# Kernel tuning notes

Measured on AMD Instinct MI355X. Metric: run time of the kernel, lower is better.

Reference implementation:

```python
import jax, jax.numpy as jnp
import numpy as np

N_PATHS, N_LINKS, L, DEG, D = 50000, 10000, 8, 40, 64
ITERS = 8
# (min, scale) pairs from override_min_max_scores
MM_FT = (0.0, 1e-4); MM_FP = (0.0, 1e-3); MM_FPS = (0.0, 1e-3); MM_LC = (0.0, 1e-5)


def _gru(x, h, wx, wh, bx, bh):
    # Keras GRUCell (reset_after=True, tanh/sigmoid)
    mx = x @ wx + bx
    mh = h @ wh + bh
    xz, xr, xh = jnp.split(mx, 3, axis=-1)
    rz, rr, rh = jnp.split(mh, 3, axis=-1)
    z = jax.nn.sigmoid(xz + rz)
    r = jax.nn.sigmoid(xr + rr)
    hh = jnp.tanh(xh + r * rh)
    return z * h + (1.0 - z) * hh


def setup_inputs():
    key = jax.random.key(0)
    ks = jax.random.split(key, 30)
    w = lambda k, s: jax.random.normal(k, s, jnp.float32) * 0.05
    inp = {
        'flow_traffic': jax.random.uniform(ks[0], (N_PATHS, 1), jnp.float32, 100.0, 10000.0),
        'flow_packets': jax.random.uniform(ks[1], (N_PATHS, 1), jnp.float32, 1.0, 1000.0),
        'flow_packet_size': jax.random.uniform(ks[2], (N_PATHS, 1), jnp.float32, 100.0, 1500.0),
        'link_capacity': jax.random.uniform(ks[3], (N_LINKS, 1), jnp.float32, 1.0, 100.0),
        'link_to_path': jax.random.randint(ks[4], (N_PATHS, L), 0, N_LINKS, jnp.int32),
        'path_to_link': jnp.stack([
            jax.random.randint(ks[5], (N_LINKS, DEG), 0, N_PATHS, jnp.int32),
            jax.random.randint(ks[6], (N_LINKS, DEG), 1, L + 1, jnp.int32)], axis=-1),
        'pe_w1': w(ks[7], (3, D)), 'pe_b1': jnp.zeros((D,), jnp.float32),
        'pe_w2': w(ks[8], (D, D)), 'pe_b2': jnp.zeros((D,), jnp.float32),
        'le_w1': w(ks[9], (2, D)), 'le_b1': jnp.zeros((D,), jnp.float32),
        'le_w2': w(ks[10], (D, D)), 'le_b2': jnp.zeros((D,), jnp.float32),
        'pg_wx': w(ks[11], (D, 3 * D)), 'pg_wh': w(ks[12], (D, 3 * D)),
        'pg_bx': jnp.zeros((3 * D,), jnp.float32), 'pg_bh': jnp.zeros((3 * D,), jnp.float32),
        'lg_wx': w(ks[13], (D, 3 * D)), 'lg_wh': w(ks[14], (D, 3 * D)),
        'lg_bx': jnp.zeros((3 * D,), jnp.float32), 'lg_bh': jnp.zeros((3 * D,), jnp.float32),
        'ro_w1': w(ks[15], (D, D // 2)), 'ro_b1': jnp.zeros((D // 2,), jnp.float32),
        'ro_w2': w(ks[16], (D // 2, D // 4)), 'ro_b2': jnp.zeros((D // 4,), jnp.float32),
        'ro_w3': w(ks[17], (D // 4, 1)), 'ro_b3': jnp.zeros((1,), jnp.float32),
    }
    return inp


def reference(flow_traffic, flow_packets, flow_packet_size, link_capacity, link_to_path, path_to_link,
              pe_w1, pe_b1, pe_w2, pe_b2, le_w1, le_b1, le_w2, le_b2,
              pg_wx, pg_wh, pg_bx, pg_bh, lg_wx, lg_wh, lg_bx, lg_bh,
              ro_w1, ro_b1, ro_w2, ro_b2, ro_w3, ro_b3):
    # per-link load: sum of traffic of paths crossing the link / capacity
    load = flow_traffic[path_to_link[:, :, 0], 0].sum(axis=1, keepdims=True) / (link_capacity * 1e9)
    # initial embeddings (min-max scaled features)
    pe_in = jnp.concatenate([(flow_traffic - MM_FT[0]) * MM_FT[1],
                             (flow_packets - MM_FP[0]) * MM_FP[1],
                             (flow_packet_size - MM_FPS[0]) * MM_FPS[1]], axis=1)
    path_state = jax.nn.relu(jax.nn.relu(pe_in @ pe_w1 + pe_b1) @ pe_w2 + pe_b2)  # [n_paths, D]
    le_in = jnp.concatenate([(link_capacity - MM_LC[0]) * MM_LC[1], load], axis=1)
    link_state = jax.nn.relu(jax.nn.relu(le_in @ le_w1 + le_b1) @ le_w2 + le_b2)  # [n_links, D]

    path_state_sequence = None
    for _ in range(ITERS):
        link_gather = link_state[link_to_path]  # [n_paths, L, D]
        prev = path_state

        def step(h, x_t):
            h2 = _gru(x_t, h, pg_wx, pg_wh, pg_bx, pg_bh)
            return h2, h2

        path_state, seq = jax.lax.scan(step, path_state, jnp.swapaxes(link_gather, 0, 1))
        path_state_sequence = jnp.concatenate([prev[:, None], jnp.swapaxes(seq, 0, 1)], axis=1)  # [n_paths, L+1, D]
        # gather_nd over (path index, position in path) then sum per link
        path_gather = path_state_sequence[path_to_link[:, :, 0], path_to_link[:, :, 1]]  # [n_links, DEG, D]
        path_sum = path_gather.sum(axis=1)  # [n_links, D]
        link_state = _gru(path_sum, link_state, lg_wx, lg_wh, lg_bx, lg_bh)

    h = jax.nn.relu(path_state_sequence[:, 1:] @ ro_w1 + ro_b1)
    h = jax.nn.relu(h @ ro_w2 + ro_b2)
    occupancy = jax.nn.softplus(h @ ro_w3 + ro_b3)  # [n_paths, L, 1]
    capacity_gather = link_capacity[link_to_path]  # [n_paths, L, 1]
    delay = (occupancy / capacity_gather).sum(axis=1)  # [n_paths, 1]
    return delay
```

## Files before the change

### kernel.cpp

```cpp
#include <hip/hip_runtime.h>
#include <math.h>

#define N_PATHS 50000
#define N_LINKS 10000
#define LPATH   8
#define DEG     40
#define DIM     64
#define G3      192
#define ITERS   8
#define ROF_OFF (4*24*512)

typedef float f32x4  __attribute__((ext_vector_type(4)));
typedef short bf16x8 __attribute__((ext_vector_type(8)));

__device__ __forceinline__ float fsigmoid(float x){
  return __builtin_amdgcn_rcpf(1.0f + __expf(-x));
}
__device__ __forceinline__ float ftanh(float x){
  return 1.0f - 2.0f*__builtin_amdgcn_rcpf(__expf(2.0f*x) + 1.0f);
}
__device__ __forceinline__ unsigned short bf16_rne(float v){
  unsigned u = __float_as_uint(v);
  return (unsigned short)((u + 0x7FFFu + ((u>>16)&1u)) >> 16);
}
__device__ __forceinline__ unsigned pack_bf16(float a, float b){
  unsigned r;
  asm("v_cvt_pk_bf16_f32 %0, %1, %2" : "=v"(r) : "v"(a), "v"(b));
  return r;
}
__device__ __forceinline__ float lo16f(unsigned v){ return __uint_as_float(v << 16); }
__device__ __forceinline__ float hi16f(unsigned v){ return __uint_as_float(v & 0xFFFF0000u); }
__device__ __forceinline__ void split8(const float* s, bf16x8& hi, bf16x8& lo){
  #pragma unroll
  for (int e=0;e<8;e++){
    unsigned short hb = bf16_rne(s[e]);
    float lof = s[e] - __uint_as_float(((unsigned)hb)<<16);
    hi[e] = (short)hb; lo[e] = (short)bf16_rne(lof);
  }
}
__device__ __forceinline__ void accum8(float* a, uint4 v){
  unsigned x[4] = {v.x, v.y, v.z, v.w};
  #pragma unroll
  for (int q=0;q<4;q++){
    a[2*q]   += __uint_as_float((x[q]&0xFFFFu)<<16);
    a[2*q+1] += __uint_as_float(x[q]&0xFFFF0000u);
  }
}

__global__ __launch_bounds__(256) void path_embed(
    const float* __restrict__ ft, const float* __restrict__ fp, const float* __restrict__ fps,
    const float* __restrict__ w1, const float* __restrict__ b1,
    const float* __restrict__ w2, const float* __restrict__ b2,
    float* __restrict__ path_state)
{
  __shared__ float h1[4][DIM];
  int j  = threadIdx.x & 63;
  int pl = threadIdx.x >> 6;
  int p  = blockIdx.x*4 + pl;
  float x0 = ft[p]*1e-4f, x1 = fp[p]*1e-3f, x2 = fps[p]*1e-3f;
  float h = b1[j] + x0*w1[0*DIM+j] + x1*w1[1*DIM+j] + x2*w1[2*DIM+j];
  h1[pl][j] = fmaxf(h, 0.f);
  __syncthreads();
  float acc = b2[j];
  #pragma unroll 8
  for (int k=0;k<DIM;k++) acc = fmaf(h1[pl][k], w2[k*DIM+j], acc);
  path_state[p*DIM+j] = fmaxf(acc, 0.f);
}

__global__ __launch_bounds__(256) void link_embed(
    const float* __restrict__ ft, const float* __restrict__ cap, const int* __restrict__ ptl,
    const float* __restrict__ w1, const float* __restrict__ b1,
    const float* __restrict__ w2, const float* __restrict__ b2,
    float* __restrict__ link_state)
{
  __shared__ float h1[4][DIM];
  int j  = threadIdx.x & 63;
  int wl = threadIdx.x >> 6;
  int l  = blockIdx.x*4 + wl;
  float s = 0.f;
  if (j < DEG) s = ft[ptl[(l*DEG + j)*2 + 0]];
  #pragma unroll
  for (int off=32; off; off>>=1) s += __shfl_down(s, off);
  float load = __shfl(s, 0) / (cap[l]*1e9f);
  float x0 = cap[l]*1e-5f;
  float h = b1[j] + x0*w1[0*DIM+j] + load*w1[1*DIM+j];
  h1[wl][j] = fmaxf(h, 0.f);
  __syncthreads();
  float acc = b2[j];
  #pragma unroll 8
  for (int k=0;k<DIM;k++) acc = fmaf(h1[wl][k], w2[k*DIM+j], acc);
  link_state[l*DIM+j] = fmaxf(acc, 0.f);
}

__global__ __launch_bounds__(256) void pack_frags(
    const float* __restrict__ pg_wh, const float* __restrict__ pg_wx,
    const float* __restrict__ lg_wx, const float* __restrict__ lg_wh,
    const float* __restrict__ ro_w1, const float* __restrict__ ro_w2,
    unsigned short* __restrict__ whf)
{
  int tid = blockIdx.x*256 + threadIdx.x;
  int i = tid & 7, l = (tid>>3)&63;
  if (tid < ROF_OFF){
    int f = (tid>>9)%24, m = tid/(24*512);
    int nt = f>>1, kc = f&1;
    int k = kc*32 + (l>>4)*8 + i;
    int n = nt*16 + (l&15);
    const float* src = (m==0)?pg_wh : (m==1)?pg_wx : (m==2)?lg_wx : lg_wh;
    whf[tid] = bf16_rne(src[k*G3 + n]);
  } else if (tid < ROF_OFF + 4*512){
    int f = (tid - ROF_OFF) >> 9;
    int nt = f>>1, kc = f&1;
    whf[tid] = bf16_rne(ro_w1[(kc*32 + (l>>4)*8 + i)*32 + nt*16 + (l&15)]);
  } else if (tid < ROF_OFF + 5*512){
    whf[tid] = bf16_rne(ro_w2[((l>>4)*8 + i)*16 + (l&15)]);
  }
}

__global__ __launch_bounds__(192) void compute_lx(
    const float* __restrict__ link_state, const float* __restrict__ wx,
    const float* __restrict__ bx, const float* __restrict__ bh,
    unsigned short* __restrict__ LXq)
{
  __shared__ float ls[4][DIM];
  int g  = threadIdx.x;
  int l0 = blockIdx.x*4;
  if (g < DIM){
    #pragma unroll
    for (int li=0; li<4; li++) ls[li][g] = link_state[(l0+li)*DIM+g];
  }
  __syncthreads();
  float b = bx[g] + (g < 128 ? bh[g] : 0.f);
  float a0=b, a1=b, a2=b, a3=b;
  #pragma unroll 8
  for (int k=0;k<DIM;k++){
    float w = wx[k*G3+g];
    a0 = fmaf(ls[0][k], w, a0);
    a1 = fmaf(ls[1][k], w, a1);
    a2 = fmaf(ls[2][k], w, a2);
    a3 = fmaf(ls[3][k], w, a3);
  }
  int comp = g >> 6, dim = g & 63;
  int pos = dim*3 + comp;
  LXq[(size_t)(l0+0)*G3+pos]=bf16_rne(a0);
  LXq[(size_t)(l0+1)*G3+pos]=bf16_rne(a1);
  LXq[(size_t)(l0+2)*G3+pos]=bf16_rne(a2);
  LXq[(size_t)(l0+3)*G3+pos]=bf16_rne(a3);
}

__global__ __launch_bounds__(256) void path_scan_mfma(
    const unsigned short* __restrict__ LXq, const int* __restrict__ ltp,
    const unsigned short* __restrict__ whf, const float* __restrict__ bh,
    float* __restrict__ path_state, unsigned short* __restrict__ seq16)
{
  __shared__ __align__(16) unsigned short htile[2][16*72];
  __shared__ int ltps[128];
  int tid = threadIdx.x, l = tid & 63, w = tid >> 6;
  int lg = l >> 4, lr = l & 15;
  int p0 = blockIdx.x*16;

  bf16x8 bf[3][2];
  #pragma unroll
  for (int j=0;j<3;j++){
    int nt = w + j*4;
    bf[j][0] = *(const bf16x8*)(whf + (size_t)(nt*2+0)*512 + l*8);
    bf[j][1] = *(const bf16x8*)(whf + (size_t)(nt*2+1)*512 + l*8);
  }
  float bhq[4];
  #pragma unroll
  for (int r=0;r<4;r++) bhq[r] = bh[128 + w*16 + lg*4 + r];

  if (tid < 128) ltps[tid] = ltp[(size_t)p0*LPATH + tid];

  {
    int pi = tid >> 4, c4 = (tid & 15)*4;
    float4 v = *(const float4*)(path_state + (size_t)(p0+pi)*DIM + c4);
    uint2 u = make_uint2(pack_bf16(v.x, v.y), pack_bf16(v.z, v.w));
    *(uint2*)&htile[0][pi*72 + c4] = u;
  }
  f32x4 hold = *(const f32x4*)(path_state + (size_t)(p0+lr)*DIM + w*16 + lg*4);

  __syncthreads();

  unsigned short* seqp = seq16 + ((size_t)(p0+lr)*LPATH)*DIM + w*16 + lg*4;
  const size_t dimoff = (size_t)(w*16 + lg*4)*3;
  int cur = 0;

  uint2 c0, c1, c2;
  {
    const unsigned short* x = LXq + (size_t)ltps[lr*LPATH]*G3 + dimoff;
    c0 = *(const uint2*)x; c1 = *(const uint2*)(x+4); c2 = *(const uint2*)(x+8);
  }

  for (int t=0; t<LPATH; t++){
    int tn = (t < LPATH-1) ? t+1 : t;
    const unsigned short* xn = LXq + (size_t)ltps[lr*LPATH + tn]*G3 + dimoff;
    uint2 n0 = *(const uint2*)xn, n1 = *(const uint2*)(xn+4), n2 = *(const uint2*)(xn+8);

    bf16x8 h0 = *(const bf16x8*)&htile[cur][lr*72 +  0 + lg*8];
    bf16x8 h1 = *(const bf16x8*)&htile[cur][lr*72 + 32 + lg*8];
    f32x4 accz = (f32x4){0.f,0.f,0.f,0.f};
    f32x4 accr = (f32x4){0.f,0.f,0.f,0.f};
    f32x4 accq = (f32x4){bhq[0],bhq[1],bhq[2],bhq[3]};
    accz = __builtin_amdgcn_mfma_f32_16x16x32_bf16(bf[0][0], h0, accz, 0,0,0);
    accr = __builtin_amdgcn_mfma_f32_16x16x32_bf16(bf[1][0], h0, accr, 0,0,0);
    accq = __builtin_amdgcn_mfma_f32_16x16x32_bf16(bf[2][0], h0, accq, 0,0,0);
    accz = __builtin_amdgcn_mfma_f32_16x16x32_bf16(bf[0][1], h1, accz, 0,0,0);
    accr = __builtin_amdgcn_mfma_f32_16x16x32_bf16(bf[1][1], h1, accr, 0,0,0);
    accq = __builtin_amdgcn_mfma_f32_16x16x32_bf16(bf[2][1], h1, accq, 0,0,0);

    float lz[4]  = { lo16f(c0.x), hi16f(c0.y), lo16f(c1.y), hi16f(c2.x) };
    float lrr[4] = { hi16f(c0.x), lo16f(c1.x), hi16f(c1.y), lo16f(c2.y) };
    float lq[4]  = { lo16f(c0.y), hi16f(c1.x), lo16f(c2.x), hi16f(c2.y) };
    f32x4 hn;
    #pragma unroll
    for (int r=0;r<4;r++){
      float z  = fsigmoid(lz[r]  + accz[r]);
      float rr = fsigmoid(lrr[r] + accr[r]);
      float hh = ftanh(lq[r] + rr*accq[r]);
      hn[r] = fmaf(z, hold[r]-hh, hh);
    }
    hold = hn;
    uint2 u = make_uint2(pack_bf16(hn[0], hn[1]), pack_bf16(hn[2], hn[3]));
    *(uint2*)&htile[cur^1][lr*72 + w*16 + lg*4] = u;
    *(uint2*)(seqp + (size_t)t*DIM) = u;
    __syncthreads();
    cur ^= 1;
    c0 = n0; c1 = n1; c2 = n2;
  }
  *(f32x4*)(path_state + (size_t)(p0+lr)*DIM + w*16 + lg*4) = hold;
}

__global__ __launch_bounds__(256) void link_fused(
    const unsigned short* __restrict__ seq16, const int* __restrict__ ptl,
    const unsigned short* __restrict__ whf,
    const float* __restrict__ lbx, const float* __restrict__ lbh,
    const float* __restrict__ pbx, const float* __restrict__ pbh,
    float* __restrict__ link_state, unsigned short* __restrict__ LXq)
{
  __shared__ float pspart[4][16][64];
  __shared__ float tile[16*68];
  int tid = threadIdx.x, l = tid & 63, w = tid >> 6;
  int lr = l & 15, lg = l >> 4;
  int l0 = blockIdx.x*16;

  float ps[16];
  #pragma unroll
  for (int i=0;i<16;i++) ps[i]=0.f;
  {
    const int* pe = ptl + (size_t)(l0+lr)*DEG*2 + w*10*2;
    #pragma unroll
    for (int d=0; d<10; d++){
      int pp = pe[2*d], tt = pe[2*d+1];
      const unsigned short* rowp = seq16 + ((size_t)pp*LPATH + (tt-1))*DIM;
      accum8(ps,   *(const uint4*)(rowp + lg*8));
      accum8(ps+8, *(const uint4*)(rowp + 32 + lg*8));
    }
  }
  #pragma unroll
  for (int i=0;i<16;i++) pspart[w][i][l] = ps[i];
  __syncthreads();

  #pragma unroll
  for (int i=0;i<16;i++)
    ps[i] = pspart[0][i][l] + pspart[1][i][l] + pspart[2][i][l] + pspart[3][i][l];

  bf16x8 phi[2], plo[2], lhi[2], llo[2];
  #pragma unroll
  for (int kc=0;kc<2;kc++){
    split8(ps + kc*8, phi[kc], plo[kc]);
    float hs[8];
    const float* lsr = link_state + (size_t)(l0+lr)*DIM + kc*32 + lg*8;
    *(f32x4*)hs = *(const f32x4*)lsr;
    *(f32x4*)(hs+4) = *(const f32x4*)(lsr+4);
    split8(hs, lhi[kc], llo[kc]);
  }
  f32x4 mxa[3], mha[3];
  #pragma unroll
  for (int j=0;j<3;j++){
    int nt = w + j*4;
    float bxv = lbx[nt*16+lr], bhv = lbh[nt*16+lr];
    mxa[j] = (f32x4){bxv,bxv,bxv,bxv};
    mha[j] = (f32x4){bhv,bhv,bhv,bhv};
    #pragma unroll
    for (int kc=0;kc<2;kc++){
      bf16x8 bwx = *(const bf16x8*)(whf + (size_t)((2*24 + nt*2+kc)*512) + l*8);
      mxa[j] = __builtin_amdgcn_mfma_f32_16x16x32_bf16(phi[kc], bwx, mxa[j], 0,0,0);
      mxa[j] = __builtin_amdgcn_mfma_f32_16x16x32_bf16(plo[kc], bwx, mxa[j], 0,0,0);
      bf16x8 bwh = *(const bf16x8*)(whf + (size_t)((3*24 + nt*2+kc)*512) + l*8);
      mha[j] = __builtin_amdgcn_mfma_f32_16x16x32_bf16(lhi[kc], bwh, mha[j], 0,0,0);
      mha[j] = __builtin_amdgcn_mfma_f32_16x16x32_bf16(llo[kc], bwh, mha[j], 0,0,0);
    }
  }
  __syncthreads();

  #pragma unroll
  for (int r=0;r<4;r++){
    size_t lk = (size_t)(l0 + lg*4 + r)*DIM + w*16 + lr;
    float lsv = link_state[lk];
    float z  = fsigmoid(mxa[0][r] + mha[0][r]);
    float rr = fsigmoid(mxa[1][r] + mha[1][r]);
    float hh = ftanh(mxa[2][r] + rr*mha[2][r]);
    float hn = fmaf(z, lsv-hh, hh);
    link_state[lk] = hn;
    tile[(lg*4+r)*68 + w*16 + lr] = hn;
  }
  __syncthreads();

  f32x4 lxa[3];
  #pragma unroll
  for (int j=0;j<3;j++){
    int g = (w + j*4)*16 + lr;
    float b = pbx[g] + (g < 128 ? pbh[g] : 0.f);
    lxa[j] = (f32x4){b,b,b,b};
  }
  #pragma unroll
  for (int kc=0;kc<2;kc++){
    float hs[8];
    #pragma unroll
    for (int i=0;i<8;i++) hs[i] = tile[lr*68 + kc*32 + lg*8 + i];
    bf16x8 thi, tlo; split8(hs, thi, tlo);
    #pragma unroll
    for (int j=0;j<3;j++){
      int nt = w + j*4;
      bf16x8 bw = *(const bf16x8*)(whf + (size_t)((1*24 + nt*2+kc)*512) + l*8);
      lxa[j] = __builtin_amdgcn_mfma_f32_16x16x32_bf16(thi, bw, lxa[j], 0,0,0);
      lxa[j] = __builtin_amdgcn_mfma_f32_16x16x32_bf16(tlo, bw, lxa[j], 0,0,0);
    }
  }
  #pragma unroll
  for (int r=0;r<4;r++){
    int link = l0 + lg*4 + r;
    size_t base = (size_t)link*G3 + (size_t)(w*16 + lr)*3;
    LXq[base+0] = bf16_rne(lxa[0][r]);
    LXq[base+1] = bf16_rne(lxa[1][r]);
    LXq[base+2] = bf16_rne(lxa[2][r]);
  }
}

__global__ __launch_bounds__(256) void readout(
    const unsigned short* __restrict__ seq16, const int* __restrict__ ltp,
    const float* __restrict__ cap, const unsigned short* __restrict__ whf,
    const float* __restrict__ b1, const float* __restrict__ b2,
    const float* __restrict__ w3, const float* __restrict__ b3,
    float* __restrict__ out)
{
  __shared__ __align__(16) unsigned short tr[4][2][16*40];
  int tid = threadIdx.x, l = tid & 63, w = tid >> 6;
  int lg = l >> 4, lr = l & 15;
  size_t wbase = (size_t)blockIdx.x*256 + (size_t)w*64;
  if (wbase >= (size_t)N_PATHS*LPATH) return;

  const unsigned short* rof = whf + ROF_OFF;
  bf16x8 w1f[2][2], w2f;
  #pragma unroll
  for (int nt=0;nt<2;nt++)
    #pragma unroll
    for (int kc=0;kc<2;kc++)
      w1f[nt][kc] = *(const bf16x8*)(rof + (size_t)(nt*2+kc)*512 + l*8);
  w2f = *(const bf16x8*)(rof + (size_t)4*512 + l*8);
  float b1a = b1[lr], b1b = b1[16+lr], b2v = b2[lr], w3v = w3[lr], b3v = b3[0];

  bf16x8 a0[4], a1[4];
  #pragma unroll
  for (int tt=0;tt<4;tt++){
    const unsigned short* ap = seq16 + (wbase + tt*16 + lr)*DIM + lg*8;
    a0[tt] = *(const bf16x8*)ap;
    a1[tt] = *(const bf16x8*)(ap + 32);
  }

  #pragma unroll
  for (int tt=0;tt<4;tt++){
    size_t rowbase = wbase + tt*16;
    f32x4 acc1a = (f32x4){b1a,b1a,b1a,b1a};
    f32x4 acc1b = (f32x4){b1b,b1b,b1b,b1b};
    acc1a = __builtin_amdgcn_mfma_f32_16x16x32_bf16(a0[tt], w1f[0][0], acc1a, 0,0,0);
    acc1a = __builtin_amdgcn_mfma_f32_16x16x32_bf16(a1[tt], w1f[0][1], acc1a, 0,0,0);
    acc1b = __builtin_amdgcn_mfma_f32_16x16x32_bf16(a0[tt], w1f[1][0], acc1b, 0,0,0);
    acc1b = __builtin_amdgcn_mfma_f32_16x16x32_bf16(a1[tt], w1f[1][1], acc1b, 0,0,0);
    unsigned short* trw = tr[w][tt&1];
    #pragma unroll
    for (int r=0;r<4;r++){
      int row = lg*4 + r;
      trw[row*40 + lr]      = bf16_rne(fmaxf(acc1a[r], 0.f));
      trw[row*40 + 16 + lr] = bf16_rne(fmaxf(acc1b[r], 0.f));
    }
    bf16x8 a2 = *(const bf16x8*)&trw[lr*40 + lg*8];
    f32x4 acc2 = (f32x4){b2v,b2v,b2v,b2v};
    acc2 = __builtin_amdgcn_mfma_f32_16x16x32_bf16(a2, w2f, acc2, 0,0,0);
    f32x4 val;
    #pragma unroll
    for (int r=0;r<4;r++) val[r] = fmaxf(acc2[r], 0.f) * w3v;
    #pragma unroll
    for (int off=1; off<16; off<<=1){
      #pragma unroll
      for (int r=0;r<4;r++) val[r] += __shfl_xor(val[r], off);
    }
    float dsum = 0.f;
    #pragma unroll
    for (int r=0;r<4;r++){
      size_t grow = rowbase + lg*4 + r;
      float o = val[r] + b3v;
      float sp = (o > 20.f) ? o : log1pf(__expf(o));
      dsum += sp * __builtin_amdgcn_rcpf(cap[ltp[grow]]);
    }
    dsum += __shfl_xor(dsum, 16);
    if (lr == 0 && (lg & 1) == 0)
      out[(rowbase >> 3) + (lg >> 1)] = dsum;
  }
}

extern "C" void kernel_launch(void* const* d_in, const int* in_sizes, int n_in,
                              void* d_out, int out_size, void* d_ws, size_t ws_size,
                              hipStream_t stream) {
  const float* ft    = (const float*)d_in[0];
  const float* fpk   = (const float*)d_in[1];
  const float* fps   = (const float*)d_in[2];
  const float* cap   = (const float*)d_in[3];
  const int*   ltp   = (const int*)  d_in[4];
  const int*   ptl   = (const int*)  d_in[5];
  const float* pe_w1 = (const float*)d_in[6];
  const float* pe_b1 = (const float*)d_in[7];
  const float* pe_w2 = (const float*)d_in[8];
  const float* pe_b2 = (const float*)d_in[9];
  const float* le_w1 = (const float*)d_in[10];
  const float* le_b1 = (const float*)d_in[11];
  const float* le_w2 = (const float*)d_in[12];
  const float* le_b2 = (const float*)d_in[13];
  const float* pg_wx = (const float*)d_in[14];
  const float* pg_wh = (const float*)d_in[15];
  const float* pg_bx = (const float*)d_in[16];
  const float* pg_bh = (const float*)d_in[17];
  const float* lg_wx = (const float*)d_in[18];
  const float* lg_wh = (const float*)d_in[19];
  const float* lg_bx = (const float*)d_in[20];
  const float* lg_bh = (const float*)d_in[21];
  const float* ro_w1 = (const float*)d_in[22];
  const float* ro_b1 = (const float*)d_in[23];
  const float* ro_w2 = (const float*)d_in[24];
  const float* ro_b2 = (const float*)d_in[25];
  const float* ro_w3 = (const float*)d_in[26];
  const float* ro_b3 = (const float*)d_in[27];
  float* out = (float*)d_out;

  float* path_state = (float*)d_ws;
  float* link_state = path_state + (size_t)N_PATHS*DIM;
  unsigned short* LXq   = (unsigned short*)(link_state + (size_t)N_LINKS*DIM);
  unsigned short* seq16 = LXq + (size_t)N_LINKS*G3;
  unsigned short* whf   = seq16 + (size_t)N_PATHS*LPATH*DIM;

  path_embed<<<N_PATHS/4, 256, 0, stream>>>(ft, fpk, fps, pe_w1, pe_b1, pe_w2, pe_b2, path_state);
  link_embed<<<N_LINKS/4, 256, 0, stream>>>(ft, cap, ptl, le_w1, le_b1, le_w2, le_b2, link_state);
  pack_frags<<<202, 256, 0, stream>>>(pg_wh, pg_wx, lg_wx, lg_wh, ro_w1, ro_w2, whf);
  compute_lx<<<N_LINKS/4, 192, 0, stream>>>(link_state, pg_wx, pg_bx, pg_bh, LXq);
  for (int it=0; it<ITERS; ++it){
    path_scan_mfma<<<N_PATHS/16, 256, 0, stream>>>(LXq, ltp, whf, pg_bh, path_state, seq16);
    if (it < ITERS-1)
      link_fused<<<N_LINKS/16, 256, 0, stream>>>(seq16, ptl, whf,
          lg_bx, lg_bh, pg_bx, pg_bh, link_state, LXq);
  }
  readout<<<(N_PATHS*LPATH + 255)/256, 256, 0, stream>>>(seq16, ltp, cap, whf,
      ro_b1, ro_b2, ro_w3, ro_b3, out);
}
```

Measured before the change: 522.5 us.

## Give each wavefront its own 16-path GRU scan to drop block barriers

```diff
diff --git a/kernel.cpp b/kernel.cpp
--- a/kernel.cpp
+++ b/kernel.cpp
@@ -8,6 +8,7 @@
 #define DIM     64
 #define G3      192
 #define ITERS   8
+#define HP      76
 #define ROF_OFF (4*24*512)
 
 typedef float f32x4  __attribute__((ext_vector_type(4)));
@@ -152,82 +153,95 @@
     const unsigned short* __restrict__ whf, const float* __restrict__ bh,
     float* __restrict__ path_state, unsigned short* __restrict__ seq16)
 {
-  __shared__ __align__(16) unsigned short htile[2][16*72];
-  __shared__ int ltps[128];
+  __shared__ __align__(16) unsigned short bw_lds[24*512];
+  __shared__ __align__(16) unsigned short htile[4][16*HP];
+  __shared__ float bq_lds[DIM];
+  __shared__ int ltps[4][128];
   int tid = threadIdx.x, l = tid & 63, w = tid >> 6;
   int lg = l >> 4, lr = l & 15;
-  int p0 = blockIdx.x*16;
-
-  bf16x8 bf[3][2];
-  #pragma unroll
-  for (int j=0;j<3;j++){
-    int nt = w + j*4;
-    bf[j][0] = *(const bf16x8*)(whf + (size_t)(nt*2+0)*512 + l*8);
-    bf[j][1] = *(const bf16x8*)(whf + (size_t)(nt*2+1)*512 + l*8);
-  }
-  float bhq[4];
-  #pragma unroll
-  for (int r=0;r<4;r++) bhq[r] = bh[128 + w*16 + lg*4 + r];
-
-  if (tid < 128) ltps[tid] = ltp[(size_t)p0*LPATH + tid];
-
+  int g = blockIdx.x*4 + w;
+  int p0 = g*16;
+  if (p0 > N_PATHS-16) p0 = N_PATHS-16;
+
+  { const uint4* src=(const uint4*)whf; uint4* dst=(uint4*)bw_lds;
+    #pragma unroll
+    for (int i=0;i<6;i++) dst[i*256+tid] = src[i*256+tid]; }
+  if (tid < DIM) bq_lds[tid] = bh[128 + tid];
+
+  *(int2*)&ltps[w][l*2] = *(const int2*)(ltp + (size_t)p0*LPATH + l*2);
+
+  f32x4 hold[4];
+  #pragma unroll
+  for (int t4=0;t4<4;t4++){
+    hold[t4] = *(const f32x4*)(path_state + (size_t)(p0+lr)*DIM + t4*16 + lg*4);
+    uint2 u = make_uint2(pack_bf16(hold[t4][0], hold[t4][1]), pack_bf16(hold[t4][2], hold[t4][3]));
+    *(uint2*)&htile[w][lr*HP + t4*16 + lg*4] = u;
+  }
+
+  __syncthreads();
+
+  unsigned short* seqp = seq16 + ((size_t)(p0+lr)*LPATH)*DIM;
+
+  uint4 cA[4]; uint2 cB[4];
   {
-    int pi = tid >> 4, c4 = (tid & 15)*4;
-    float4 v = *(const float4*)(path_state + (size_t)(p0+pi)*DIM + c4);
-    uint2 u = make_uint2(pack_bf16(v.x, v.y), pack_bf16(v.z, v.w));
-    *(uint2*)&htile[0][pi*72 + c4] = u;
-  }
-  f32x4 hold = *(const f32x4*)(path_state + (size_t)(p0+lr)*DIM + w*16 + lg*4);
-
-  __syncthreads();
-
-  unsigned short* seqp = seq16 + ((size_t)(p0+lr)*LPATH)*DIM + w*16 + lg*4;
-  const size_t dimoff = (size_t)(w*16 + lg*4)*3;
-  int cur = 0;
-
-  uint2 c0, c1, c2;
-  {
-    const unsigned short* x = LXq + (size_t)ltps[lr*LPATH]*G3 + dimoff;
-    c0 = *(const uint2*)x; c1 = *(const uint2*)(x+4); c2 = *(const uint2*)(x+8);
+    const unsigned short* lx = LXq + (size_t)ltps[w][lr*LPATH]*G3;
+    #pragma unroll
+    for (int t4=0;t4<4;t4++){
+      cA[t4] = *(const uint4*)(lx + t4*48 + lg*12);
+      cB[t4] = *(const uint2*)(lx + t4*48 + lg*12 + 8);
+    }
   }
 
   for (int t=0; t<LPATH; t++){
     int tn = (t < LPATH-1) ? t+1 : t;
-    const unsigned short* xn = LXq + (size_t)ltps[lr*LPATH + tn]*G3 + dimoff;
-    uint2 n0 = *(const uint2*)xn, n1 = *(const uint2*)(xn+4), n2 = *(const uint2*)(xn+8);
-
-    bf16x8 h0 = *(const bf16x8*)&htile[cur][lr*72 +  0 + lg*8];
-    bf16x8 h1 = *(const bf16x8*)&htile[cur][lr*72 + 32 + lg*8];
-    f32x4 accz = (f32x4){0.f,0.f,0.f,0.f};
-    f32x4 accr = (f32x4){0.f,0.f,0.f,0.f};
-    f32x4 accq = (f32x4){bhq[0],bhq[1],bhq[2],bhq[3]};
-    accz = __builtin_amdgcn_mfma_f32_16x16x32_bf16(bf[0][0], h0, accz, 0,0,0);
-    accr = __builtin_amdgcn_mfma_f32_16x16x32_bf16(bf[1][0], h0, accr, 0,0,0);
-    accq = __builtin_amdgcn_mfma_f32_16x16x32_bf16(bf[2][0], h0, accq, 0,0,0);
-    accz = __builtin_amdgcn_mfma_f32_16x16x32_bf16(bf[0][1], h1, accz, 0,0,0);
-    accr = __builtin_amdgcn_mfma_f32_16x16x32_bf16(bf[1][1], h1, accr, 0,0,0);
-    accq = __builtin_amdgcn_mfma_f32_16x16x32_bf16(bf[2][1], h1, accq, 0,0,0);
-
-    float lz[4]  = { lo16f(c0.x), hi16f(c0.y), lo16f(c1.y), hi16f(c2.x) };
-    float lrr[4] = { hi16f(c0.x), lo16f(c1.x), hi16f(c1.y), lo16f(c2.y) };
-    float lq[4]  = { lo16f(c0.y), hi16f(c1.x), lo16f(c2.x), hi16f(c2.y) };
-    f32x4 hn;
-    #pragma unroll
-    for (int r=0;r<4;r++){
-      float z  = fsigmoid(lz[r]  + accz[r]);
-      float rr = fsigmoid(lrr[r] + accr[r]);
-      float hh = ftanh(lq[r] + rr*accq[r]);
-      hn[r] = fmaf(z, hold[r]-hh, hh);
-    }
-    hold = hn;
-    uint2 u = make_uint2(pack_bf16(hn[0], hn[1]), pack_bf16(hn[2], hn[3]));
-    *(uint2*)&htile[cur^1][lr*72 + w*16 + lg*4] = u;
-    *(uint2*)(seqp + (size_t)t*DIM) = u;
-    __syncthreads();
-    cur ^= 1;
-    c0 = n0; c1 = n1; c2 = n2;
-  }
-  *(f32x4*)(path_state + (size_t)(p0+lr)*DIM + w*16 + lg*4) = hold;
+    const unsigned short* lxn = LXq + (size_t)ltps[w][lr*LPATH + tn]*G3;
+    uint4 nA[4]; uint2 nB[4];
+    #pragma unroll
+    for (int t4=0;t4<4;t4++){
+      nA[t4] = *(const uint4*)(lxn + t4*48 + lg*12);
+      nB[t4] = *(const uint2*)(lxn + t4*48 + lg*12 + 8);
+    }
+
+    bf16x8 h0 = *(const bf16x8*)&htile[w][lr*HP +  0 + lg*8];
+    bf16x8 h1 = *(const bf16x8*)&htile[w][lr*HP + 32 + lg*8];
+    f32x4 acc[12];
+    #pragma unroll
+    for (int nt=0;nt<8;nt++) acc[nt] = (f32x4){0.f,0.f,0.f,0.f};
+    #pragma unroll
+    for (int t4=0;t4<4;t4++) acc[8+t4] = *(const f32x4*)&bq_lds[t4*16 + lg*4];
+    #pragma unroll
+    for (int nt=0;nt<12;nt++){
+      bf16x8 w0 = *(const bf16x8*)&bw_lds[(nt*2+0)*512 + l*8];
+      acc[nt] = __builtin_amdgcn_mfma_f32_16x16x32_bf16(w0, h0, acc[nt], 0,0,0);
+      bf16x8 w1 = *(const bf16x8*)&bw_lds[(nt*2+1)*512 + l*8];
+      acc[nt] = __builtin_amdgcn_mfma_f32_16x16x32_bf16(w1, h1, acc[nt], 0,0,0);
+    }
+
+    #pragma unroll
+    for (int t4=0;t4<4;t4++){
+      uint4 v0 = cA[t4]; uint2 v1 = cB[t4];
+      float lz[4]  = { lo16f(v0.x), hi16f(v0.y), lo16f(v0.w), hi16f(v1.x) };
+      float lrr[4] = { hi16f(v0.x), lo16f(v0.z), hi16f(v0.w), lo16f(v1.y) };
+      float lq[4]  = { lo16f(v0.y), hi16f(v0.z), lo16f(v1.x), hi16f(v1.y) };
+      f32x4 hn;
+      #pragma unroll
+      for (int r=0;r<4;r++){
+        float z  = fsigmoid(lz[r]  + acc[t4][r]);
+        float rr = fsigmoid(lrr[r] + acc[4+t4][r]);
+        float hh = ftanh(lq[r] + rr*acc[8+t4][r]);
+        hn[r] = fmaf(z, hold[t4][r]-hh, hh);
+      }
+      hold[t4] = hn;
+      uint2 u = make_uint2(pack_bf16(hn[0], hn[1]), pack_bf16(hn[2], hn[3]));
+      *(uint2*)&htile[w][lr*HP + t4*16 + lg*4] = u;
+      *(uint2*)(seqp + (size_t)t*DIM + t4*16 + lg*4) = u;
+    }
+    #pragma unroll
+    for (int t4=0;t4<4;t4++){ cA[t4] = nA[t4]; cB[t4] = nB[t4]; }
+  }
+  #pragma unroll
+  for (int t4=0;t4<4;t4++)
+    *(f32x4*)(path_state + (size_t)(p0+lr)*DIM + t4*16 + lg*4) = hold[t4];
 }
 
 __global__ __launch_bounds__(256) void link_fused(
@@ -453,7 +467,7 @@
   pack_frags<<<202, 256, 0, stream>>>(pg_wh, pg_wx, lg_wx, lg_wh, ro_w1, ro_w2, whf);
   compute_lx<<<N_LINKS/4, 192, 0, stream>>>(link_state, pg_wx, pg_bx, pg_bh, LXq);
   for (int it=0; it<ITERS; ++it){
-    path_scan_mfma<<<N_PATHS/16, 256, 0, stream>>>(LXq, ltp, whf, pg_bh, path_state, seq16);
+    path_scan_mfma<<<(N_PATHS/16 + 3)/4, 256, 0, stream>>>(LXq, ltp, whf, pg_bh, path_state, seq16);
     if (it < ITERS-1)
       link_fused<<<N_LINKS/16, 256, 0, stream>>>(seq16, ptl, whf,
           lg_bx, lg_bh, pg_bx, pg_bh, link_state, LXq);
```

Result: slower. 575.2 us (+10.1%).
